# Performance work log

Hardware: AMD Instinct MI355X
Metric: run time of the kernel (lower is better)

The kernel has to match this reference:

```python
import jax, jax.numpy as jnp
from jax import lax
import numpy as np

B, S, D, H = 256, 2048, 16, 128
HH = H // 2  # head hidden = 64


def _p(key, shape, scale=0.05):
    return scale * jax.random.normal(key, shape, dtype=jnp.float32)


def setup_inputs() -> dict:
    key = jax.random.key(0)
    ks = jax.random.split(key, 12)
    return {
        "x": jax.random.normal(ks[0], (B, S, D), dtype=jnp.float32),
        # LSTM layer 0 (PyTorch gate order: i, f, g, o along the 4H axis)
        "W_ih0": _p(ks[1], (4 * H, D)),
        "W_hh0": _p(ks[2], (4 * H, H)),
        "b_ih0": jnp.zeros((4 * H,), jnp.float32),
        "b_hh0": jnp.zeros((4 * H,), jnp.float32),
        # LSTM layer 1
        "W_ih1": _p(ks[3], (4 * H, H)),
        "W_hh1": _p(ks[4], (4 * H, H)),
        "b_ih1": jnp.zeros((4 * H,), jnp.float32),
        "b_hh1": jnp.zeros((4 * H,), jnp.float32),
        # return head: Linear(H, H//2) -> LeakyReLU -> Linear(H//2, 1)
        "Wr1": _p(ks[5], (HH, H)), "br1": jnp.zeros((HH,), jnp.float32),
        "Wr2": _p(ks[6], (1, HH)), "br2": jnp.zeros((1,), jnp.float32),
        # vol head: Linear -> LeakyReLU -> Linear -> Softplus
        "Wv1": _p(ks[7], (HH, H)), "bv1": jnp.zeros((HH,), jnp.float32),
        "Wv2": _p(ks[8], (1, HH)), "bv2": jnp.zeros((1,), jnp.float32),
    }


def _lstm_layer(x, W_ih, W_hh, b_ih, b_hh):
    # x: (B, S, Din) -> hs: (B, S, H); PyTorch gate order i, f, g, o
    b, s, _ = x.shape
    h_dim = W_hh.shape[1]
    xg = jnp.einsum('bsd,gd->bsg', x, W_ih) + (b_ih + b_hh)  # (B, S, 4H)

    def step(carry, xg_t):
        h, c = carry
        g = xg_t + h @ W_hh.T
        i, f, gc, o = jnp.split(g, 4, axis=-1)
        i = jax.nn.sigmoid(i)
        f = jax.nn.sigmoid(f)
        gc = jnp.tanh(gc)
        o = jax.nn.sigmoid(o)
        c = f * c + i * gc
        h = o * jnp.tanh(c)
        return (h, c), h

    h0 = jnp.zeros((b, h_dim), x.dtype)
    (hN, cN), hs = lax.scan(step, (h0, jnp.zeros_like(h0)), jnp.swapaxes(xg, 0, 1))
    return jnp.swapaxes(hs, 0, 1), hN, cN


def reference(x, W_ih0, W_hh0, b_ih0, b_hh0, W_ih1, W_hh1, b_ih1, b_hh1,
              Wr1, br1, Wr2, br2, Wv1, bv1, Wv2, bv2):
    h1, hN0, cN0 = _lstm_layer(x, W_ih0, W_hh0, b_ih0, b_hh0)
    # inter-layer dropout is inactive at inference (eval mode)
    h2, hN1, cN1 = _lstm_layer(h1, W_ih1, W_hh1, b_ih1, b_hh1)
    # return head
    r = jax.nn.leaky_relu(jnp.einsum('bsh,kh->bsk', h2, Wr1) + br1)
    returns = jnp.einsum('bsk,ok->bso', r, Wr2) + br2
    # volatility head
    v = jax.nn.leaky_relu(jnp.einsum('bsh,kh->bsk', h2, Wv1) + bv1)
    volatility = jax.nn.softplus(jnp.einsum('bsk,ok->bso', v, Wv2) + bv2)
    hidden_h = jnp.stack([hN0, hN1], axis=0)  # (num_layers, B, H)
    hidden_c = jnp.stack([cN0, cN1], axis=0)
    return returns, volatility, hidden_h, hidden_c
```

## Files before the change

kernel.cpp:

```cpp
#include <hip/hip_runtime.h>
#include <hip/hip_bf16.h>

#define B_ 256
#define S_ 2048
#define D_ 16
#define H_ 128

typedef unsigned int u32;
typedef unsigned short u16;
typedef _Float16 h2t __attribute__((ext_vector_type(2)));

#define RET0 ((size_t)0)
#define VOL0 ((size_t)524288)
#define HH0  ((size_t)1048576)
#define HC0  ((size_t)1114112)

__device__ __forceinline__ float fdot2(u32 a, u32 b, float c) {
    return __builtin_amdgcn_fdot2(__builtin_bit_cast(h2t, a),
                                  __builtin_bit_cast(h2t, b), c, false);
}
__device__ __forceinline__ u32 packh2(float a, float b) {
    h2t h; h[0] = (_Float16)a; h[1] = (_Float16)b;
    return __builtin_bit_cast(u32, h);
}
__device__ __forceinline__ float sigm(float x) {
    return __builtin_amdgcn_rcpf(1.f + __builtin_amdgcn_exp2f(-1.44269504f * x));
}
__device__ __forceinline__ float tanh_(float x) {
    return 2.f * __builtin_amdgcn_rcpf(1.f + __builtin_amdgcn_exp2f(-2.88539008f * x)) - 1.f;
}
__device__ __forceinline__ float softplus_(float x) {
    if (x > 20.f) return x;
    const float e = __builtin_amdgcn_exp2f(1.44269504f * x);
    return 0.69314718f * __builtin_amdgcn_logf(1.f + e);
}

__global__ __launch_bounds__(512) void k_l0(
    const float* __restrict__ x, const float* __restrict__ Wih,
    const float* __restrict__ Whh, const float* __restrict__ bih,
    const float* __restrict__ bhh, u32* __restrict__ h1out,
    float* __restrict__ out)
{
    __shared__ float xs[512 * 16];
    __shared__ float gates[4][128];
    __shared__ float hf[128];
    __shared__ u32 och[64 * 64];

    const int tid = threadIdx.x, b = blockIdx.x;
    const int g = tid >> 7, m = tid & 127, row = g * 128 + m;

    float wx[16], wh[128];
#pragma unroll
    for (int j = 0; j < 16; ++j) wx[j] = Wih[row * 16 + j];
#pragma unroll
    for (int j = 0; j < 128; ++j) wh[j] = Whh[row * 128 + j];
    const float bs = bih[row] + bhh[row];

    float c = 0.f;
    if (tid < 128) hf[tid] = 0.f;
    __syncthreads();

    const float* xb = x + (size_t)b * S_ * D_;
    for (int t = 0; t < S_; ++t) {
        if ((t & 511) == 0) {
            for (int i = tid; i < 2048; i += 512) {
                const float4 v = *(const float4*)(xb + (size_t)t * 16 + i * 4);
                *(float4*)(&xs[i * 4]) = v;
            }
            __syncthreads();
        }
        float a = bs;
        const float* xt = &xs[(t & 511) * 16];
#pragma unroll
        for (int j = 0; j < 16; ++j) a += wx[j] * xt[j];
#pragma unroll
        for (int j = 0; j < 128; ++j) a += wh[j] * hf[j];
        gates[g][m] = a;
        __syncthreads();
        if (tid < 128) {
            const float ig = sigm(gates[0][tid]);
            const float fg = sigm(gates[1][tid]);
            const float gc = tanh_(gates[2][tid]);
            const float og = sigm(gates[3][tid]);
            c = fg * c + ig * gc;
            const float h = og * tanh_(c);
            hf[tid] = h;
            if (t == S_ - 1) {
                out[HH0 + (size_t)b * H_ + tid] = h;
                out[HC0 + (size_t)b * H_ + tid] = c;
            }
        }
        __syncthreads();
        if (tid < 64) och[(t & 63) * 64 + tid] = packh2(hf[2 * tid], hf[2 * tid + 1]);
        if ((t & 63) == 63) {
            __syncthreads();
            u32* dst = h1out + ((size_t)b * S_ + (t - 63)) * 64;
            *(uint4*)(dst + tid * 8)     = *(const uint4*)(&och[tid * 8]);
            *(uint4*)(dst + tid * 8 + 4) = *(const uint4*)(&och[tid * 8 + 4]);
        }
        __syncthreads();
    }
}

__global__ __launch_bounds__(512) void k_l1(
    u32* __restrict__ hws,
    const float* __restrict__ Wih, const float* __restrict__ Whh,
    const float* __restrict__ bih, const float* __restrict__ bhh,
    float* __restrict__ out)
{
    __shared__ u32 h1w[128 * 64];
    __shared__ float gates[4][128];
    __shared__ u32 hp[64];
    __shared__ u32 och[64 * 64];

    const int tid = threadIdx.x, b = blockIdx.x;
    const int g = tid >> 7, m = tid & 127, row = g * 128 + m;

    u32 wi[64], wh[64];
#pragma unroll
    for (int j = 0; j < 64; ++j) {
        const float2 a = *(const float2*)(Wih + row * 128 + 2 * j);
        const float2 cc = *(const float2*)(Whh + row * 128 + 2 * j);
        wi[j] = packh2(a.x, a.y);
        wh[j] = packh2(cc.x, cc.y);
    }
    const float bs = bih[row] + bhh[row];

    float c = 0.f;
    if (tid < 64) hp[tid] = 0u;
    __syncthreads();

    u32* hb = hws + (size_t)b * S_ * 64;
    for (int t = 0; t < S_; ++t) {
        if ((t & 127) == 0) {
            for (int i = tid; i < 2048; i += 512)
                *(uint4*)(&h1w[i * 4]) = *(const uint4*)(hb + (size_t)t * 64 + i * 4);
            __syncthreads();
        }
        float a = bs;
        const u32* h1t = &h1w[(t & 127) * 64];
#pragma unroll
        for (int j = 0; j < 64; ++j) a = fdot2(h1t[j], wi[j], a);
#pragma unroll
        for (int j = 0; j < 64; ++j) a = fdot2(hp[j], wh[j], a);
        gates[g][m] = a;
        __syncthreads();
        if (tid < 128) {
            const float ig = sigm(gates[0][tid]);
            const float fg = sigm(gates[1][tid]);
            const float gc = tanh_(gates[2][tid]);
            const float og = sigm(gates[3][tid]);
            c = fg * c + ig * gc;
            const float h = og * tanh_(c);
            ((u16*)hp)[tid] = __builtin_bit_cast(unsigned short, (_Float16)h);
            if (t == S_ - 1) {
                out[HH0 + 32768 + (size_t)b * H_ + tid] = h;
                out[HC0 + 32768 + (size_t)b * H_ + tid] = c;
            }
        }
        __syncthreads();
        if (tid < 64) och[(t & 63) * 64 + tid] = hp[tid];
        if ((t & 63) == 63) {
            __syncthreads();
            u32* dst = hb + (size_t)(t - 63) * 64;
            *(uint4*)(dst + tid * 8)     = *(const uint4*)(&och[tid * 8]);
            *(uint4*)(dst + tid * 8 + 4) = *(const uint4*)(&och[tid * 8 + 4]);
        }
        __syncthreads();
    }
}

__global__ __launch_bounds__(256) void k_heads(
    const u32* __restrict__ h2p,
    const float* __restrict__ Wr1, const float* __restrict__ br1,
    const float* __restrict__ Wr2, const float* __restrict__ br2,
    const float* __restrict__ Wv1, const float* __restrict__ bv1,
    const float* __restrict__ Wv2, const float* __restrict__ bv2,
    float* __restrict__ out)
{
    __shared__ u32 wr[64 * 64], wv[64 * 64];
    __shared__ float w2r[64], w2v[64], b1r[64], b1v[64];

    const int tid = threadIdx.x;
    for (int i = tid; i < 4096; i += 256) {
        wr[i] = packh2(Wr1[2 * i], Wr1[2 * i + 1]);
        wv[i] = packh2(Wv1[2 * i], Wv1[2 * i + 1]);
    }
    if (tid < 64) {
        w2r[tid] = Wr2[tid]; w2v[tid] = Wv2[tid];
        b1r[tid] = br1[tid]; b1v[tid] = bv1[tid];
    }
    __syncthreads();

    const size_t bs = (size_t)blockIdx.x * 256 + tid;
    u32 hq[64];
    const u32* src = h2p + bs * 64;
#pragma unroll
    for (int j4 = 0; j4 < 16; ++j4) {
        const uint4 v = *(const uint4*)(src + j4 * 4);
        hq[j4 * 4] = v.x; hq[j4 * 4 + 1] = v.y; hq[j4 * 4 + 2] = v.z; hq[j4 * 4 + 3] = v.w;
    }
    float ret = br2[0], vol = bv2[0];
    for (int k = 0; k < 64; ++k) {
        float r = b1r[k], v = b1v[k];
#pragma unroll
        for (int j = 0; j < 64; ++j) r = fdot2(hq[j], wr[k * 64 + j], r);
#pragma unroll
        for (int j = 0; j < 64; ++j) v = fdot2(hq[j], wv[k * 64 + j], v);
        r = r > 0.f ? r : 0.01f * r;
        v = v > 0.f ? v : 0.01f * v;
        ret += r * w2r[k];
        vol += v * w2v[k];
    }
    out[RET0 + bs] = ret;
    out[VOL0 + bs] = softplus_(vol);
}

extern "C" void kernel_launch(void* const* d_in, const int* in_sizes, int n_in,
                              void* d_out, int out_size, void* d_ws, size_t ws_size,
                              hipStream_t stream) {
    (void)in_sizes; (void)n_in; (void)out_size; (void)ws_size;
    const float* x    = (const float*)d_in[0];
    const float* Wih0 = (const float*)d_in[1];
    const float* Whh0 = (const float*)d_in[2];
    const float* bih0 = (const float*)d_in[3];
    const float* bhh0 = (const float*)d_in[4];
    const float* Wih1 = (const float*)d_in[5];
    const float* Whh1 = (const float*)d_in[6];
    const float* bih1 = (const float*)d_in[7];
    const float* bhh1 = (const float*)d_in[8];
    const float* Wr1  = (const float*)d_in[9];
    const float* br1  = (const float*)d_in[10];
    const float* Wr2  = (const float*)d_in[11];
    const float* br2  = (const float*)d_in[12];
    const float* Wv1  = (const float*)d_in[13];
    const float* bv1  = (const float*)d_in[14];
    const float* Wv2  = (const float*)d_in[15];
    const float* bv2  = (const float*)d_in[16];
    u32* hws = (u32*)d_ws;
    float* out = (float*)d_out;

    k_l0<<<B_, 512, 0, stream>>>(x, Wih0, Whh0, bih0, bhh0, hws, out);
    k_l1<<<B_, 512, 0, stream>>>(hws, Wih1, Whh1, bih1, bhh1, out);
    k_heads<<<2048, 256, 0, stream>>>(hws, Wr1, br1, Wr2, br2, Wv1, bv1, Wv2, bv2, out);
}
```

Measured before the change: 4.117 ms.

## Split gate rows across 8-lane groups, shuffle-reduce gates, cut barriers per step

```diff
diff --git a/kernel.cpp b/kernel.cpp
--- a/kernel.cpp
+++ b/kernel.cpp
@@ -35,138 +35,180 @@
     return 0.69314718f * __builtin_amdgcn_logf(1.f + e);
 }
 
-__global__ __launch_bounds__(512) void k_l0(
+__global__ __launch_bounds__(1024, 4) void k_l0(
     const float* __restrict__ x, const float* __restrict__ Wih,
     const float* __restrict__ Whh, const float* __restrict__ bih,
     const float* __restrict__ bhh, u32* __restrict__ h1out,
     float* __restrict__ out)
 {
-    __shared__ float xs[512 * 16];
-    __shared__ float gates[4][128];
-    __shared__ float hf[128];
-    __shared__ u32 och[64 * 64];
+    __shared__ u32 xp2[2][4096];
+    __shared__ u32 hb[2][64];
+    __shared__ u32 och[4096];
 
     const int tid = threadIdx.x, b = blockIdx.x;
-    const int g = tid >> 7, m = tid & 127, row = g * 128 + m;
-
-    float wx[16], wh[128];
-#pragma unroll
-    for (int j = 0; j < 16; ++j) wx[j] = Wih[row * 16 + j];
-#pragma unroll
-    for (int j = 0; j < 128; ++j) wh[j] = Whh[row * 128 + j];
-    const float bs = bih[row] + bhh[row];
-
+    const int m = tid >> 3, g = (tid >> 1) & 3, k0 = tid & 1;
+    const int row = g * H_ + m;
+
+    u32 w[36];
+    {
+        const float* p1 = k0 ? (Whh + row * H_ + 56) : (Wih + row * D_);
+        const float* p2 = k0 ? (Whh + row * H_ + 72) : (Whh + row * H_);
+#pragma unroll
+        for (int j = 0; j < 4; ++j) {
+            const float4 f = ((const float4*)p1)[j];
+            w[2 * j] = packh2(f.x, f.y); w[2 * j + 1] = packh2(f.z, f.w);
+        }
+#pragma unroll
+        for (int j = 0; j < 14; ++j) {
+            const float4 f = ((const float4*)p2)[j];
+            w[8 + 2 * j] = packh2(f.x, f.y); w[9 + 2 * j] = packh2(f.z, f.w);
+        }
+    }
+    const float bs = k0 ? 0.f : (bih[row] + bhh[row]);
+
+    const float* xb = x + (size_t)b * S_ * D_;
+    for (int i = tid; i < 2048; i += 1024) {
+        const float4 v = *(const float4*)(xb + i * 4);
+        xp2[0][2 * i] = packh2(v.x, v.y);
+        xp2[0][2 * i + 1] = packh2(v.z, v.w);
+    }
+    if (tid < 128) ((u32*)hb)[tid] = 0u;
     float c = 0.f;
-    if (tid < 128) hf[tid] = 0.f;
     __syncthreads();
 
-    const float* xb = x + (size_t)b * S_ * D_;
     for (int t = 0; t < S_; ++t) {
-        if ((t & 511) == 0) {
-            for (int i = tid; i < 2048; i += 512) {
-                const float4 v = *(const float4*)(xb + (size_t)t * 16 + i * 4);
-                *(float4*)(&xs[i * 4]) = v;
+        if ((t & 511) == 0 && t < S_ - 512) {
+            const int nw = (t >> 9) + 1;
+            u32* dst = xp2[nw & 1];
+            const float* src = xb + (size_t)nw * 8192;
+            for (int i = tid; i < 2048; i += 1024) {
+                const float4 v = *(const float4*)(src + i * 4);
+                dst[2 * i] = packh2(v.x, v.y);
+                dst[2 * i + 1] = packh2(v.z, v.w);
             }
+        }
+        const u32* hprev = hb[(t + 1) & 1];
+        const u32* xslot = &xp2[(t >> 9) & 1][(t & 511) * 8];
+        const uint4* pA = (const uint4*)(k0 ? hprev + 28 : xslot);
+        const uint4* pB = (const uint4*)(k0 ? hprev + 36 : hprev);
+
+        float a0 = bs, a1 = 0.f, a2 = 0.f, a3 = 0.f;
+        {
+            const uint4 v0 = pA[0], v1 = pA[1];
+            a0 = fdot2(v0.x, w[0], a0); a1 = fdot2(v0.y, w[1], a1);
+            a2 = fdot2(v0.z, w[2], a2); a3 = fdot2(v0.w, w[3], a3);
+            a0 = fdot2(v1.x, w[4], a0); a1 = fdot2(v1.y, w[5], a1);
+            a2 = fdot2(v1.z, w[6], a2); a3 = fdot2(v1.w, w[7], a3);
+        }
+#pragma unroll
+        for (int p = 0; p < 7; ++p) {
+            const uint4 v = pB[p];
+            a0 = fdot2(v.x, w[8 + 4 * p], a0); a1 = fdot2(v.y, w[9 + 4 * p], a1);
+            a2 = fdot2(v.z, w[10 + 4 * p], a2); a3 = fdot2(v.w, w[11 + 4 * p], a3);
+        }
+        float a = (a0 + a1) + (a2 + a3);
+        a += __shfl_xor(a, 1);
+        const float af = __shfl_down(a, 2);
+        const float ag = __shfl_down(a, 4);
+        const float ao = __shfl_down(a, 6);
+        float hv = 0.f;
+        if ((tid & 7) == 0) {
+            const float ig = sigm(a), fg = sigm(af);
+            const float gc = tanh_(ag), og = sigm(ao);
+            c = fg * c + ig * gc;
+            hv = og * tanh_(c);
+        }
+        const float hnb = __shfl_down(hv, 8);
+        if ((tid & 15) == 0) {
+            const u32 pp = packh2(hv, hnb);
+            hb[t & 1][m >> 1] = pp;
+            och[(t & 63) * 64 + (m >> 1)] = pp;
+        }
+        if (t == S_ - 1 && (tid & 7) == 0) {
+            out[HH0 + (size_t)b * H_ + m] = hv;
+            out[HC0 + (size_t)b * H_ + m] = c;
+        }
+        __syncthreads();
+        if ((t & 63) == 63) {
+            u32* dst = h1out + ((size_t)b * S_ + (t - 63)) * 64;
+            *(uint4*)(dst + tid * 4) = *(const uint4*)(&och[tid * 4]);
             __syncthreads();
         }
-        float a = bs;
-        const float* xt = &xs[(t & 511) * 16];
-#pragma unroll
-        for (int j = 0; j < 16; ++j) a += wx[j] * xt[j];
-#pragma unroll
-        for (int j = 0; j < 128; ++j) a += wh[j] * hf[j];
-        gates[g][m] = a;
-        __syncthreads();
-        if (tid < 128) {
-            const float ig = sigm(gates[0][tid]);
-            const float fg = sigm(gates[1][tid]);
-            const float gc = tanh_(gates[2][tid]);
-            const float og = sigm(gates[3][tid]);
-            c = fg * c + ig * gc;
-            const float h = og * tanh_(c);
-            hf[tid] = h;
-            if (t == S_ - 1) {
-                out[HH0 + (size_t)b * H_ + tid] = h;
-                out[HC0 + (size_t)b * H_ + tid] = c;
-            }
-        }
-        __syncthreads();
-        if (tid < 64) och[(t & 63) * 64 + tid] = packh2(hf[2 * tid], hf[2 * tid + 1]);
-        if ((t & 63) == 63) {
-            __syncthreads();
-            u32* dst = h1out + ((size_t)b * S_ + (t - 63)) * 64;
-            *(uint4*)(dst + tid * 8)     = *(const uint4*)(&och[tid * 8]);
-            *(uint4*)(dst + tid * 8 + 4) = *(const uint4*)(&och[tid * 8 + 4]);
-        }
-        __syncthreads();
-    }
-}
-
-__global__ __launch_bounds__(512) void k_l1(
+    }
+}
+
+__global__ __launch_bounds__(1024, 4) void k_l1(
     u32* __restrict__ hws,
     const float* __restrict__ Wih, const float* __restrict__ Whh,
     const float* __restrict__ bih, const float* __restrict__ bhh,
     float* __restrict__ out)
 {
-    __shared__ u32 h1w[128 * 64];
-    __shared__ float gates[4][128];
-    __shared__ u32 hp[64];
-    __shared__ u32 och[64 * 64];
+    __shared__ u32 h1w[8192];
+    __shared__ u32 hp[2][64];
+    __shared__ u32 och[4096];
 
     const int tid = threadIdx.x, b = blockIdx.x;
-    const int g = tid >> 7, m = tid & 127, row = g * 128 + m;
-
-    u32 wi[64], wh[64];
-#pragma unroll
-    for (int j = 0; j < 64; ++j) {
-        const float2 a = *(const float2*)(Wih + row * 128 + 2 * j);
-        const float2 cc = *(const float2*)(Whh + row * 128 + 2 * j);
-        wi[j] = packh2(a.x, a.y);
-        wh[j] = packh2(cc.x, cc.y);
-    }
-    const float bs = bih[row] + bhh[row];
-
+    const int m = tid >> 3, g = (tid >> 1) & 3, k0 = tid & 1;
+    const int row = g * H_ + m;
+
+    u32 w[64];
+    {
+        const float4* ws_ = (const float4*)((k0 ? Whh : Wih) + row * H_);
+#pragma unroll
+        for (int j = 0; j < 32; ++j) {
+            const float4 f = ws_[j];
+            w[2 * j] = packh2(f.x, f.y); w[2 * j + 1] = packh2(f.z, f.w);
+        }
+    }
+    const float bs = k0 ? 0.f : (bih[row] + bhh[row]);
+
+    if (tid < 128) ((u32*)hp)[tid] = 0u;
     float c = 0.f;
-    if (tid < 64) hp[tid] = 0u;
     __syncthreads();
 
-    u32* hb = hws + (size_t)b * S_ * 64;
-    for (int t = 0; t < S_; ++t) {
-        if ((t & 127) == 0) {
-            for (int i = tid; i < 2048; i += 512)
-                *(uint4*)(&h1w[i * 4]) = *(const uint4*)(hb + (size_t)t * 64 + i * 4);
+    u32* hbase = hws + (size_t)b * S_ * 64;
+    for (int u = 0; u < S_; ++u) {
+        if ((u & 127) == 0) {
+            for (int i = tid; i < 2048; i += 1024)
+                *(uint4*)(&h1w[i * 4]) = *(const uint4*)(hbase + (size_t)u * 64 + i * 4);
             __syncthreads();
         }
-        float a = bs;
-        const u32* h1t = &h1w[(t & 127) * 64];
-#pragma unroll
-        for (int j = 0; j < 64; ++j) a = fdot2(h1t[j], wi[j], a);
-#pragma unroll
-        for (int j = 0; j < 64; ++j) a = fdot2(hp[j], wh[j], a);
-        gates[g][m] = a;
+        const uint4* src = (const uint4*)(k0 ? hp[(u + 1) & 1] : &h1w[(u & 127) * 64]);
+        float a0 = bs, a1 = 0.f, a2 = 0.f, a3 = 0.f;
+#pragma unroll
+        for (int p = 0; p < 16; ++p) {
+            const uint4 v = src[p];
+            a0 = fdot2(v.x, w[4 * p], a0); a1 = fdot2(v.y, w[4 * p + 1], a1);
+            a2 = fdot2(v.z, w[4 * p + 2], a2); a3 = fdot2(v.w, w[4 * p + 3], a3);
+        }
+        float a = (a0 + a1) + (a2 + a3);
+        a += __shfl_xor(a, 1);
+        const float af = __shfl_down(a, 2);
+        const float ag = __shfl_down(a, 4);
+        const float ao = __shfl_down(a, 6);
+        float hv = 0.f;
+        if ((tid & 7) == 0) {
+            const float ig = sigm(a), fg = sigm(af);
+            const float gc = tanh_(ag), og = sigm(ao);
+            c = fg * c + ig * gc;
+            hv = og * tanh_(c);
+        }
+        const float hnb = __shfl_down(hv, 8);
+        if ((tid & 15) == 0) {
+            const u32 pp = packh2(hv, hnb);
+            hp[u & 1][m >> 1] = pp;
+            och[(u & 63) * 64 + (m >> 1)] = pp;
+        }
+        if (u == S_ - 1 && (tid & 7) == 0) {
+            out[HH0 + 32768 + (size_t)b * H_ + m] = hv;
+            out[HC0 + 32768 + (size_t)b * H_ + m] = c;
+        }
         __syncthreads();
-        if (tid < 128) {
-            const float ig = sigm(gates[0][tid]);
-            const float fg = sigm(gates[1][tid]);
-            const float gc = tanh_(gates[2][tid]);
-            const float og = sigm(gates[3][tid]);
-            c = fg * c + ig * gc;
-            const float h = og * tanh_(c);
-            ((u16*)hp)[tid] = __builtin_bit_cast(unsigned short, (_Float16)h);
-            if (t == S_ - 1) {
-                out[HH0 + 32768 + (size_t)b * H_ + tid] = h;
-                out[HC0 + 32768 + (size_t)b * H_ + tid] = c;
-            }
-        }
-        __syncthreads();
-        if (tid < 64) och[(t & 63) * 64 + tid] = hp[tid];
-        if ((t & 63) == 63) {
+        if ((u & 63) == 63) {
+            u32* dst = hbase + (size_t)(u - 63) * 64;
+            *(uint4*)(dst + tid * 4) = *(const uint4*)(&och[tid * 4]);
             __syncthreads();
-            u32* dst = hb + (size_t)(t - 63) * 64;
-            *(uint4*)(dst + tid * 8)     = *(const uint4*)(&och[tid * 8]);
-            *(uint4*)(dst + tid * 8 + 4) = *(const uint4*)(&och[tid * 8 + 4]);
-        }
-        __syncthreads();
+        }
     }
 }
 
@@ -240,7 +282,7 @@
     u32* hws = (u32*)d_ws;
     float* out = (float*)d_out;
 
-    k_l0<<<B_, 512, 0, stream>>>(x, Wih0, Whh0, bih0, bhh0, hws, out);
-    k_l1<<<B_, 512, 0, stream>>>(hws, Wih1, Whh1, bih1, bhh1, out);
+    k_l0<<<B_, 1024, 0, stream>>>(x, Wih0, Whh0, bih0, bhh0, hws, out);
+    k_l1<<<B_, 1024, 0, stream>>>(hws, Wih1, Whh1, bih1, bhh1, out);
     k_heads<<<2048, 256, 0, stream>>>(hws, Wr1, br1, Wr2, br2, Wv1, bv1, Wv2, bv2, out);
 }
```

Measured after the change: 5.058 ms. +22.8%, slower.

## Batch LSTM recurrences across 16 sequences per block using MFMA

Applied to the files above, without the earlier changes.

```diff
diff --git a/kernel.cpp b/kernel.cpp
--- a/kernel.cpp
+++ b/kernel.cpp
@@ -9,19 +9,25 @@
 typedef unsigned int u32;
 typedef unsigned short u16;
 typedef _Float16 h2t __attribute__((ext_vector_type(2)));
+typedef _Float16 f16x8 __attribute__((ext_vector_type(8)));
+typedef float f32x4 __attribute__((ext_vector_type(4)));
 
 #define RET0 ((size_t)0)
 #define VOL0 ((size_t)524288)
 #define HH0  ((size_t)1048576)
 #define HC0  ((size_t)1114112)
 
-__device__ __forceinline__ float fdot2(u32 a, u32 b, float c) {
-    return __builtin_amdgcn_fdot2(__builtin_bit_cast(h2t, a),
-                                  __builtin_bit_cast(h2t, b), c, false);
-}
+#define MFMA16(a, b, c) __builtin_amdgcn_mfma_f32_16x16x32_f16(a, b, c, 0, 0, 0)
+
 __device__ __forceinline__ u32 packh2(float a, float b) {
     h2t h; h[0] = (_Float16)a; h[1] = (_Float16)b;
     return __builtin_bit_cast(u32, h);
+}
+__device__ __forceinline__ f16x8 pk8(float4 a, float4 b) {
+    f16x8 r;
+    r[0] = (_Float16)a.x; r[1] = (_Float16)a.y; r[2] = (_Float16)a.z; r[3] = (_Float16)a.w;
+    r[4] = (_Float16)b.x; r[5] = (_Float16)b.y; r[6] = (_Float16)b.z; r[7] = (_Float16)b.w;
+    return r;
 }
 __device__ __forceinline__ float sigm(float x) {
     return __builtin_amdgcn_rcpf(1.f + __builtin_amdgcn_exp2f(-1.44269504f * x));
@@ -34,139 +40,185 @@
     const float e = __builtin_amdgcn_exp2f(1.44269504f * x);
     return 0.69314718f * __builtin_amdgcn_logf(1.f + e);
 }
-
-__global__ __launch_bounds__(512) void k_l0(
+__device__ __forceinline__ float4 ld4(const float* p) { return *(const float4*)p; }
+
+
+__global__ __launch_bounds__(512, 2) void k_l0m(
     const float* __restrict__ x, const float* __restrict__ Wih,
     const float* __restrict__ Whh, const float* __restrict__ bih,
-    const float* __restrict__ bhh, u32* __restrict__ h1out,
+    const float* __restrict__ bhh, u32* __restrict__ hws,
     float* __restrict__ out)
 {
-    __shared__ float xs[512 * 16];
-    __shared__ float gates[4][128];
-    __shared__ float hf[128];
-    __shared__ u32 och[64 * 64];
-
-    const int tid = threadIdx.x, b = blockIdx.x;
-    const int g = tid >> 7, m = tid & 127, row = g * 128 + m;
-
-    float wx[16], wh[128];
-#pragma unroll
-    for (int j = 0; j < 16; ++j) wx[j] = Wih[row * 16 + j];
-#pragma unroll
-    for (int j = 0; j < 128; ++j) wh[j] = Whh[row * 128 + j];
-    const float bs = bih[row] + bhh[row];
-
-    float c = 0.f;
-    if (tid < 128) hf[tid] = 0.f;
+    __shared__ u32 ring[8192];
+
+    const int tid = threadIdx.x, g = blockIdx.x;
+    const int l = tid & 63, w = tid >> 6;
+    const int ub = w * 16;
+    const int col = l & 15, kg = l >> 4;
+
+    f16x8 wB[4][5];
+    float bias[4];
+#pragma unroll
+    for (int gt = 0; gt < 4; ++gt) {
+        const int n = gt * 128 + ub + col;
+        if (kg < 2) {
+            const float* p = Wih + n * 16 + kg * 8;
+            wB[gt][0] = pk8(ld4(p), ld4(p + 4));
+        } else {
+            f16x8 z = {0, 0, 0, 0, 0, 0, 0, 0};
+            wB[gt][0] = z;
+        }
+#pragma unroll
+        for (int kt = 1; kt < 5; ++kt) {
+            const float* p = Whh + n * 128 + (kt - 1) * 32 + kg * 8;
+            wB[gt][kt] = pk8(ld4(p), ld4(p + 4));
+        }
+        bias[gt] = bih[n] + bhh[n];
+    }
+
+    for (int i = tid; i < 8192; i += 512) ring[i] = 0;
+    float c1[4] = {0.f, 0.f, 0.f, 0.f};
     __syncthreads();
 
-    const float* xb = x + (size_t)b * S_ * D_;
+    const float* xrow = x + ((size_t)(g * 16 + col) * S_) * D_;
     for (int t = 0; t < S_; ++t) {
-        if ((t & 511) == 0) {
-            for (int i = tid; i < 2048; i += 512) {
-                const float4 v = *(const float4*)(xb + (size_t)t * 16 + i * 4);
-                *(float4*)(&xs[i * 4]) = v;
+        f16x8 ax = {0, 0, 0, 0, 0, 0, 0, 0};
+        if (kg < 2) {
+            const float* xp = xrow + t * 16 + kg * 8;
+            ax = pk8(ld4(xp), ld4(xp + 4));
+        }
+        f16x8 ah[4];
+        {
+            const int sl = ((t - 1) & 7) << 10;
+#pragma unroll
+            for (int kt = 0; kt < 4; ++kt)
+                ah[kt] = __builtin_bit_cast(f16x8,
+                    *(const uint4*)&ring[sl + col * 64 + (((kt * 4 + kg) ^ (col & 7)) << 2)]);
+        }
+        f32x4 acc[4];
+#pragma unroll
+        for (int gt = 0; gt < 4; ++gt) {
+            f32x4 a = {bias[gt], bias[gt], bias[gt], bias[gt]};
+            a = MFMA16(ax, wB[gt][0], a);
+#pragma unroll
+            for (int kt = 1; kt < 5; ++kt) a = MFMA16(ah[kt - 1], wB[gt][kt], a);
+            acc[gt] = a;
+        }
+#pragma unroll
+        for (int j = 0; j < 4; ++j) {
+            const float ai = acc[0][j], af = acc[1][j], ag = acc[2][j], ao = acc[3][j];
+            c1[j] = sigm(af) * c1[j] + sigm(ai) * tanh_(ag);
+            const float h = sigm(ao) * tanh_(c1[j]);
+            const u32 hp = packh2(h, __shfl_down(h, 1));
+            const int r = kg * 4 + j;
+            if (!(l & 1)) {
+                const int p = (ub + col) >> 1;
+                ring[((t & 7) << 10) + r * 64 + ((((p >> 2)) ^ (r & 7)) << 2) + (p & 3)] = hp;
+            }
+            if (t == S_ - 1) {
+                const size_t b = g * 16 + r;
+                out[HH0 + b * H_ + ub + col] = h;
+                out[HC0 + b * H_ + ub + col] = c1[j];
+            }
+        }
+        __syncthreads();
+        if ((t & 7) == 7) {
+#pragma unroll
+            for (int q = 0; q < 4; ++q) {
+                const int ch = tid * 4 + q;
+                const int s = ch >> 8, rr = (ch >> 4) & 15, cc = ch & 15;
+                const uint4 v = *(const uint4*)&ring[(s << 10) + rr * 64 + ((cc ^ (rr & 7)) << 2)];
+                *(uint4*)(hws + (((size_t)g * S_ + (t - 7 + s)) * 16 + rr) * 64 + cc * 4) = v;
             }
             __syncthreads();
         }
-        float a = bs;
-        const float* xt = &xs[(t & 511) * 16];
-#pragma unroll
-        for (int j = 0; j < 16; ++j) a += wx[j] * xt[j];
-#pragma unroll
-        for (int j = 0; j < 128; ++j) a += wh[j] * hf[j];
-        gates[g][m] = a;
-        __syncthreads();
-        if (tid < 128) {
-            const float ig = sigm(gates[0][tid]);
-            const float fg = sigm(gates[1][tid]);
-            const float gc = tanh_(gates[2][tid]);
-            const float og = sigm(gates[3][tid]);
-            c = fg * c + ig * gc;
-            const float h = og * tanh_(c);
-            hf[tid] = h;
-            if (t == S_ - 1) {
-                out[HH0 + (size_t)b * H_ + tid] = h;
-                out[HC0 + (size_t)b * H_ + tid] = c;
-            }
-        }
-        __syncthreads();
-        if (tid < 64) och[(t & 63) * 64 + tid] = packh2(hf[2 * tid], hf[2 * tid + 1]);
-        if ((t & 63) == 63) {
-            __syncthreads();
-            u32* dst = h1out + ((size_t)b * S_ + (t - 63)) * 64;
-            *(uint4*)(dst + tid * 8)     = *(const uint4*)(&och[tid * 8]);
-            *(uint4*)(dst + tid * 8 + 4) = *(const uint4*)(&och[tid * 8 + 4]);
-        }
-        __syncthreads();
-    }
-}
-
-__global__ __launch_bounds__(512) void k_l1(
+    }
+}
+
+__global__ __launch_bounds__(512, 2) void k_l1m(
     u32* __restrict__ hws,
     const float* __restrict__ Wih, const float* __restrict__ Whh,
     const float* __restrict__ bih, const float* __restrict__ bhh,
     float* __restrict__ out)
 {
-    __shared__ u32 h1w[128 * 64];
-    __shared__ float gates[4][128];
-    __shared__ u32 hp[64];
-    __shared__ u32 och[64 * 64];
-
-    const int tid = threadIdx.x, b = blockIdx.x;
-    const int g = tid >> 7, m = tid & 127, row = g * 128 + m;
-
-    u32 wi[64], wh[64];
-#pragma unroll
-    for (int j = 0; j < 64; ++j) {
-        const float2 a = *(const float2*)(Wih + row * 128 + 2 * j);
-        const float2 cc = *(const float2*)(Whh + row * 128 + 2 * j);
-        wi[j] = packh2(a.x, a.y);
-        wh[j] = packh2(cc.x, cc.y);
-    }
-    const float bs = bih[row] + bhh[row];
-
-    float c = 0.f;
-    if (tid < 64) hp[tid] = 0u;
+    __shared__ u32 ring[8192];
+
+    const int tid = threadIdx.x, g = blockIdx.x;
+    const int l = tid & 63, w = tid >> 6;
+    const int ub = w * 16;
+    const int col = l & 15, kg = l >> 4;
+
+    f16x8 wB[4][8];
+    float bias[4];
+#pragma unroll
+    for (int gt = 0; gt < 4; ++gt) {
+        const int n = gt * 128 + ub + col;
+#pragma unroll
+        for (int kt = 0; kt < 8; ++kt) {
+            const float* p = ((kt < 4) ? Wih : Whh) + n * 128 + (kt & 3) * 32 + kg * 8;
+            wB[gt][kt] = pk8(ld4(p), ld4(p + 4));
+        }
+        bias[gt] = bih[n] + bhh[n];
+    }
+
+    for (int i = tid; i < 8192; i += 512) ring[i] = 0;
+    float c2[4] = {0.f, 0.f, 0.f, 0.f};
     __syncthreads();
 
-    u32* hb = hws + (size_t)b * S_ * 64;
-    for (int t = 0; t < S_; ++t) {
-        if ((t & 127) == 0) {
-            for (int i = tid; i < 2048; i += 512)
-                *(uint4*)(&h1w[i * 4]) = *(const uint4*)(hb + (size_t)t * 64 + i * 4);
+    for (int u = 0; u < S_; ++u) {
+        f16x8 a1[4];
+        {
+            const u32* hrow = hws + (((size_t)g * S_ + u) * 16 + col) * 64;
+#pragma unroll
+            for (int kt = 0; kt < 4; ++kt)
+                a1[kt] = __builtin_bit_cast(f16x8, *(const uint4*)(hrow + kt * 16 + kg * 4));
+        }
+        f16x8 a2[4];
+        {
+            const int sl = ((u - 1) & 7) << 10;
+#pragma unroll
+            for (int kt = 0; kt < 4; ++kt)
+                a2[kt] = __builtin_bit_cast(f16x8,
+                    *(const uint4*)&ring[sl + col * 64 + (((kt * 4 + kg) ^ (col & 7)) << 2)]);
+        }
+        f32x4 acc[4];
+#pragma unroll
+        for (int gt = 0; gt < 4; ++gt) {
+            f32x4 a = {bias[gt], bias[gt], bias[gt], bias[gt]};
+#pragma unroll
+            for (int kt = 0; kt < 4; ++kt) a = MFMA16(a1[kt], wB[gt][kt], a);
+#pragma unroll
+            for (int kt = 4; kt < 8; ++kt) a = MFMA16(a2[kt - 4], wB[gt][kt], a);
+            acc[gt] = a;
+        }
+#pragma unroll
+        for (int j = 0; j < 4; ++j) {
+            const float ai = acc[0][j], af = acc[1][j], ag = acc[2][j], ao = acc[3][j];
+            c2[j] = sigm(af) * c2[j] + sigm(ai) * tanh_(ag);
+            const float h = sigm(ao) * tanh_(c2[j]);
+            const u32 hp = packh2(h, __shfl_down(h, 1));
+            const int r = kg * 4 + j;
+            if (!(l & 1)) {
+                const int p = (ub + col) >> 1;
+                ring[((u & 7) << 10) + r * 64 + ((((p >> 2)) ^ (r & 7)) << 2) + (p & 3)] = hp;
+            }
+            if (u == S_ - 1) {
+                const size_t b = g * 16 + r;
+                out[HH0 + 32768 + b * H_ + ub + col] = h;
+                out[HC0 + 32768 + b * H_ + ub + col] = c2[j];
+            }
+        }
+        __syncthreads();
+        if ((u & 7) == 7) {
+#pragma unroll
+            for (int q = 0; q < 4; ++q) {
+                const int ch = tid * 4 + q;
+                const int s = ch >> 8, rr = (ch >> 4) & 15, cc = ch & 15;
+                const uint4 v = *(const uint4*)&ring[(s << 10) + rr * 64 + ((cc ^ (rr & 7)) << 2)];
+                *(uint4*)(hws + (((size_t)g * S_ + (u - 7 + s)) * 16 + rr) * 64 + cc * 4) = v;
+            }
             __syncthreads();
         }
-        float a = bs;
-        const u32* h1t = &h1w[(t & 127) * 64];
-#pragma unroll
-        for (int j = 0; j < 64; ++j) a = fdot2(h1t[j], wi[j], a);
-#pragma unroll
-        for (int j = 0; j < 64; ++j) a = fdot2(hp[j], wh[j], a);
-        gates[g][m] = a;
-        __syncthreads();
-        if (tid < 128) {
-            const float ig = sigm(gates[0][tid]);
-            const float fg = sigm(gates[1][tid]);
-            const float gc = tanh_(gates[2][tid]);
-            const float og = sigm(gates[3][tid]);
-            c = fg * c + ig * gc;
-            const float h = og * tanh_(c);
-            ((u16*)hp)[tid] = __builtin_bit_cast(unsigned short, (_Float16)h);
-            if (t == S_ - 1) {
-                out[HH0 + 32768 + (size_t)b * H_ + tid] = h;
-                out[HC0 + 32768 + (size_t)b * H_ + tid] = c;
-            }
-        }
-        __syncthreads();
-        if (tid < 64) och[(t & 63) * 64 + tid] = hp[tid];
-        if ((t & 63) == 63) {
-            __syncthreads();
-            u32* dst = hb + (size_t)(t - 63) * 64;
-            *(uint4*)(dst + tid * 8)     = *(const uint4*)(&och[tid * 8]);
-            *(uint4*)(dst + tid * 8 + 4) = *(const uint4*)(&och[tid * 8 + 4]);
-        }
-        __syncthreads();
     }
 }
 
@@ -192,9 +244,13 @@
     }
     __syncthreads();
 
-    const size_t bs = (size_t)blockIdx.x * 256 + tid;
+    const int g = blockIdx.x >> 7;
+    const int s = (blockIdx.x & 127) * 16 + (tid >> 4);
+    const int r = tid & 15;
+    const int b = g * 16 + r;
+
     u32 hq[64];
-    const u32* src = h2p + bs * 64;
+    const u32* src = h2p + (((size_t)g * S_ + s) * 16 + r) * 64;
 #pragma unroll
     for (int j4 = 0; j4 < 16; ++j4) {
         const uint4 v = *(const uint4*)(src + j4 * 4);
@@ -202,18 +258,21 @@
     }
     float ret = br2[0], vol = bv2[0];
     for (int k = 0; k < 64; ++k) {
-        float r = b1r[k], v = b1v[k];
-#pragma unroll
-        for (int j = 0; j < 64; ++j) r = fdot2(hq[j], wr[k * 64 + j], r);
-#pragma unroll
-        for (int j = 0; j < 64; ++j) v = fdot2(hq[j], wv[k * 64 + j], v);
-        r = r > 0.f ? r : 0.01f * r;
-        v = v > 0.f ? v : 0.01f * v;
-        ret += r * w2r[k];
-        vol += v * w2v[k];
-    }
-    out[RET0 + bs] = ret;
-    out[VOL0 + bs] = softplus_(vol);
+        float rr = b1r[k], vv = b1v[k];
+#pragma unroll
+        for (int j = 0; j < 64; ++j) {
+            rr = __builtin_amdgcn_fdot2(__builtin_bit_cast(h2t, hq[j]),
+                                        __builtin_bit_cast(h2t, wr[k * 64 + j]), rr, false);
+            vv = __builtin_amdgcn_fdot2(__builtin_bit_cast(h2t, hq[j]),
+                                        __builtin_bit_cast(h2t, wv[k * 64 + j]), vv, false);
+        }
+        rr = rr > 0.f ? rr : 0.01f * rr;
+        vv = vv > 0.f ? vv : 0.01f * vv;
+        ret += rr * w2r[k];
+        vol += vv * w2v[k];
+    }
+    out[RET0 + (size_t)b * S_ + s] = ret;
+    out[VOL0 + (size_t)b * S_ + s] = softplus_(vol);
 }
 
 extern "C" void kernel_launch(void* const* d_in, const int* in_sizes, int n_in,
@@ -237,10 +296,11 @@
     const float* bv1  = (const float*)d_in[14];
     const float* Wv2  = (const float*)d_in[15];
     const float* bv2  = (const float*)d_in[16];
-    u32* hws = (u32*)d_ws;
+    u32* hws  = (u32*)d_ws;
     float* out = (float*)d_out;
 
-    k_l0<<<B_, 512, 0, stream>>>(x, Wih0, Whh0, bih0, bhh0, hws, out);
-    k_l1<<<B_, 512, 0, stream>>>(hws, Wih1, Whh1, bih1, bhh1, out);
-    k_heads<<<2048, 256, 0, stream>>>(hws, Wr1, br1, Wr2, br2, Wv1, bv1, Wv2, bv2, out);
-}
+    k_l0m<<<16, 512, 0, stream>>>(x, Wih0, Whh0, bih0, bhh0, hws, out);
+    k_l1m<<<16, 512, 0, stream>>>(hws, Wih1, Whh1, bih1, bhh1, out);
+    k_heads<<<2048, 256, 0, stream>>>(hws, Wr1, br1, Wr2, br2,
+                                      Wv1, bv1, Wv2, bv2, out);
+}
```

Result: slower. 7.340 ms (+78.3%).

## Split LSTM gate matvec across K-slices with one barrier per step

Applied to the files above, without the earlier changes.

```diff
diff --git a/kernel.cpp b/kernel.cpp
--- a/kernel.cpp
+++ b/kernel.cpp
@@ -7,7 +7,6 @@
 #define H_ 128
 
 typedef unsigned int u32;
-typedef unsigned short u16;
 typedef _Float16 h2t __attribute__((ext_vector_type(2)));
 
 #define RET0 ((size_t)0)
@@ -34,139 +33,243 @@
     const float e = __builtin_amdgcn_exp2f(1.44269504f * x);
     return 0.69314718f * __builtin_amdgcn_logf(1.f + e);
 }
-
-__global__ __launch_bounds__(512) void k_l0(
+__device__ __forceinline__ float dnb1(float a) {
+    return __builtin_bit_cast(float, __builtin_amdgcn_update_dpp(
+        0, __builtin_bit_cast(int, a), 0xB1, 0xF, 0xF, true));
+}
+
+__global__ __launch_bounds__(512, 2) void k_l0(
     const float* __restrict__ x, const float* __restrict__ Wih,
     const float* __restrict__ Whh, const float* __restrict__ bih,
     const float* __restrict__ bhh, u32* __restrict__ h1out,
     float* __restrict__ out)
 {
-    __shared__ float xs[512 * 16];
-    __shared__ float gates[4][128];
-    __shared__ float hf[128];
-    __shared__ u32 och[64 * 64];
+    __shared__ u32 xp2[2][2048];
+    __shared__ float gates[2][4][128][4];
+    __shared__ u32 hb[8][16];
+    __shared__ u32 och[2][2048];
 
     const int tid = threadIdx.x, b = blockIdx.x;
-    const int g = tid >> 7, m = tid & 127, row = g * 128 + m;
-
-    float wx[16], wh[128];
-#pragma unroll
-    for (int j = 0; j < 16; ++j) wx[j] = Wih[row * 16 + j];
-#pragma unroll
-    for (int j = 0; j < 128; ++j) wh[j] = Whh[row * 128 + j];
-    const float bs = bih[row] + bhh[row];
-
+    const int ksl = tid >> 7, m = tid & 127;
+    const int wv = tid >> 6, j = tid & 63;
+    const int unit = (ksl << 5) + (j & 31);
+
+    u32 wx[8], wh[64];
+#pragma unroll
+    for (int g = 0; g < 4; ++g) {
+        const int row = g * H_ + m;
+        const float4 fx = *(const float4*)(Wih + row * D_ + ksl * 4);
+        wx[g * 2]     = packh2(fx.x, fx.y);
+        wx[g * 2 + 1] = packh2(fx.z, fx.w);
+        const float4* whr = (const float4*)(Whh + row * H_ + ksl * 32);
+#pragma unroll
+        for (int q = 0; q < 8; ++q) {
+            const float4 f = whr[q];
+            wh[g * 16 + 2 * q]     = packh2(f.x, f.y);
+            wh[g * 16 + 2 * q + 1] = packh2(f.z, f.w);
+        }
+    }
+    const float bias0 = bih[unit] + bhh[unit];
+    const float bias1 = bih[128 + unit] + bhh[128 + unit];
+    const float bias2 = bih[256 + unit] + bhh[256 + unit];
+    const float bias3 = bih[384 + unit] + bhh[384 + unit];
+
+    const float* xb = x + (size_t)b * S_ * D_;
+#pragma unroll
+    for (int k = 0; k < 2; ++k) {
+        const int i = tid + k * 512;
+        const float4 v = *(const float4*)(xb + i * 4);
+        xp2[0][2 * i]     = packh2(v.x, v.y);
+        xp2[0][2 * i + 1] = packh2(v.z, v.w);
+    }
+    if (tid < 128) ((u32*)hb)[tid] = 0u;
     float c = 0.f;
-    if (tid < 128) hf[tid] = 0.f;
-    __syncthreads();
-
-    const float* xb = x + (size_t)b * S_ * D_;
+    __syncthreads();
+
     for (int t = 0; t < S_; ++t) {
-        if ((t & 511) == 0) {
-            for (int i = tid; i < 2048; i += 512) {
-                const float4 v = *(const float4*)(xb + (size_t)t * 16 + i * 4);
-                *(float4*)(&xs[i * 4]) = v;
+        if ((t & 255) == 0 && t < S_ - 256) {
+            const int nw = (t >> 8) + 1;
+#pragma unroll
+            for (int k = 0; k < 2; ++k) {
+                const int i = tid + k * 512;
+                const float4 v = *(const float4*)(xb + (size_t)nw * 4096 + i * 4);
+                xp2[nw & 1][2 * i]     = packh2(v.x, v.y);
+                xp2[nw & 1][2 * i + 1] = packh2(v.z, v.w);
             }
-            __syncthreads();
-        }
-        float a = bs;
-        const float* xt = &xs[(t & 511) * 16];
-#pragma unroll
-        for (int j = 0; j < 16; ++j) a += wx[j] * xt[j];
-#pragma unroll
-        for (int j = 0; j < 128; ++j) a += wh[j] * hf[j];
-        gates[g][m] = a;
+        }
+        const uint2 xv = *(const uint2*)&xp2[(t >> 8) & 1][(t & 255) * 8 + ksl * 2];
+        const uint4* hq = (const uint4*)hb[wv];
+        const uint4 h0 = hq[0], h1 = hq[1], h2 = hq[2], h3 = hq[3];
+        float a0 = fdot2(xv.x, wx[0], 0.f); a0 = fdot2(xv.y, wx[1], a0);
+        float a1 = fdot2(xv.x, wx[2], 0.f); a1 = fdot2(xv.y, wx[3], a1);
+        float a2 = fdot2(xv.x, wx[4], 0.f); a2 = fdot2(xv.y, wx[5], a2);
+        float a3 = fdot2(xv.x, wx[6], 0.f); a3 = fdot2(xv.y, wx[7], a3);
+#define DG(vv, p)                                                              \
+        a0 = fdot2(vv, wh[p], a0);        a1 = fdot2(vv, wh[16 + (p)], a1);    \
+        a2 = fdot2(vv, wh[32 + (p)], a2); a3 = fdot2(vv, wh[48 + (p)], a3);
+        DG(h0.x, 0) DG(h0.y, 1) DG(h0.z, 2) DG(h0.w, 3)
+        DG(h1.x, 4) DG(h1.y, 5) DG(h1.z, 6) DG(h1.w, 7)
+        DG(h2.x, 8) DG(h2.y, 9) DG(h2.z, 10) DG(h2.w, 11)
+        DG(h3.x, 12) DG(h3.y, 13) DG(h3.z, 14) DG(h3.w, 15)
+#undef DG
+        float4 part; part.x = a0; part.y = a1; part.z = a2; part.w = a3;
+        *(float4*)&gates[t & 1][ksl][m][0] = part;
         __syncthreads();
-        if (tid < 128) {
-            const float ig = sigm(gates[0][tid]);
-            const float fg = sigm(gates[1][tid]);
-            const float gc = tanh_(gates[2][tid]);
-            const float og = sigm(gates[3][tid]);
-            c = fg * c + ig * gc;
-            const float h = og * tanh_(c);
-            hf[tid] = h;
-            if (t == S_ - 1) {
-                out[HH0 + (size_t)b * H_ + tid] = h;
-                out[HC0 + (size_t)b * H_ + tid] = c;
-            }
-        }
-        __syncthreads();
-        if (tid < 64) och[(t & 63) * 64 + tid] = packh2(hf[2 * tid], hf[2 * tid + 1]);
-        if ((t & 63) == 63) {
-            __syncthreads();
-            u32* dst = h1out + ((size_t)b * S_ + (t - 63)) * 64;
-            *(uint4*)(dst + tid * 8)     = *(const uint4*)(&och[tid * 8]);
-            *(uint4*)(dst + tid * 8 + 4) = *(const uint4*)(&och[tid * 8 + 4]);
-        }
-        __syncthreads();
-    }
-}
-
-__global__ __launch_bounds__(512) void k_l1(
+        if ((t & 31) == 0 && t) {
+            u32* dst = h1out + ((size_t)b * S_ + (t - 32)) * 64;
+            *(uint4*)(dst + tid * 4) = *(const uint4*)&och[((t >> 5) & 1) ^ 1][tid * 4];
+        }
+        const float4 s0 = *(const float4*)&gates[t & 1][0][unit][0];
+        const float4 s1 = *(const float4*)&gates[t & 1][1][unit][0];
+        const float4 s2 = *(const float4*)&gates[t & 1][2][unit][0];
+        const float4 s3 = *(const float4*)&gates[t & 1][3][unit][0];
+        const float ig = sigm((s0.x + s1.x) + (s2.x + s3.x) + bias0);
+        const float fg = sigm((s0.y + s1.y) + (s2.y + s3.y) + bias1);
+        const float gc = tanh_((s0.z + s1.z) + (s2.z + s3.z) + bias2);
+        const float og = sigm((s0.w + s1.w) + (s2.w + s3.w) + bias3);
+        c = fg * c + ig * gc;
+        const float h = og * tanh_(c);
+        const u32 pp = packh2(h, dnb1(h));
+        if ((j & 33) == 0) {
+            hb[wv][j >> 1] = pp;
+            if (!(wv & 1)) och[(t >> 5) & 1][(t & 31) * 64 + (unit >> 1)] = pp;
+        }
+        if (t == S_ - 1 && !(wv & 1) && j < 32) {
+            out[HH0 + (size_t)b * H_ + unit] = h;
+            out[HC0 + (size_t)b * H_ + unit] = c;
+        }
+    }
+    __syncthreads();
+    {
+        u32* dst = h1out + ((size_t)b * S_ + (S_ - 32)) * 64;
+        *(uint4*)(dst + tid * 4) = *(const uint4*)&och[1][tid * 4];
+    }
+}
+
+__global__ __launch_bounds__(512, 2) void k_l1(
     u32* __restrict__ hws,
     const float* __restrict__ Wih, const float* __restrict__ Whh,
     const float* __restrict__ bih, const float* __restrict__ bhh,
     float* __restrict__ out)
 {
-    __shared__ u32 h1w[128 * 64];
-    __shared__ float gates[4][128];
-    __shared__ u32 hp[64];
-    __shared__ u32 och[64 * 64];
+    __shared__ u32 h1w[2][5120];
+    __shared__ float gates[2][4][128][4];
+    __shared__ u32 hb[8][32];
+    __shared__ u32 och[2][2048];
 
     const int tid = threadIdx.x, b = blockIdx.x;
-    const int g = tid >> 7, m = tid & 127, row = g * 128 + m;
-
-    u32 wi[64], wh[64];
-#pragma unroll
-    for (int j = 0; j < 64; ++j) {
-        const float2 a = *(const float2*)(Wih + row * 128 + 2 * j);
-        const float2 cc = *(const float2*)(Whh + row * 128 + 2 * j);
-        wi[j] = packh2(a.x, a.y);
-        wh[j] = packh2(cc.x, cc.y);
-    }
-    const float bs = bih[row] + bhh[row];
-
+    const int ksl = tid >> 7, m = tid & 127;
+    const int wv = tid >> 6, j = tid & 63;
+    const int unit = ((ksl & 1) << 6) + j;
+
+    u32 w[128];
+    const float* Wsel = (ksl < 2) ? Wih : Whh;
+    const int eb = (ksl & 1) * 64;
+#pragma unroll
+    for (int g = 0; g < 4; ++g) {
+        const int row = g * H_ + m;
+        const float4* wr_ = (const float4*)(Wsel + row * H_ + eb);
+#pragma unroll
+        for (int q = 0; q < 16; ++q) {
+            const float4 f = wr_[q];
+            w[g * 32 + 2 * q]     = packh2(f.x, f.y);
+            w[g * 32 + 2 * q + 1] = packh2(f.z, f.w);
+        }
+    }
+    const float bias0 = bih[unit] + bhh[unit];
+    const float bias1 = bih[128 + unit] + bhh[128 + unit];
+    const float bias2 = bih[256 + unit] + bhh[256 + unit];
+    const float bias3 = bih[384 + unit] + bhh[384 + unit];
+
+    u32* hbase = hws + (size_t)b * S_ * 64;
+#pragma unroll
+    for (int k = 0; k < 2; ++k) {
+        const int i = tid + k * 512;
+        const uint4 v = *(const uint4*)(hbase + i * 4);
+        *(uint4*)&h1w[0][(i >> 4) * 80 + ((i & 15) >> 2) * 20 + (i & 3) * 4] = v;
+    }
+    if (tid < 256) ((u32*)hb)[tid] = 0u;
     float c = 0.f;
-    if (tid < 64) hp[tid] = 0u;
-    __syncthreads();
-
-    u32* hb = hws + (size_t)b * S_ * 64;
-    for (int t = 0; t < S_; ++t) {
-        if ((t & 127) == 0) {
-            for (int i = tid; i < 2048; i += 512)
-                *(uint4*)(&h1w[i * 4]) = *(const uint4*)(hb + (size_t)t * 64 + i * 4);
-            __syncthreads();
-        }
-        float a = bs;
-        const u32* h1t = &h1w[(t & 127) * 64];
-#pragma unroll
-        for (int j = 0; j < 64; ++j) a = fdot2(h1t[j], wi[j], a);
-#pragma unroll
-        for (int j = 0; j < 64; ++j) a = fdot2(hp[j], wh[j], a);
-        gates[g][m] = a;
+    __syncthreads();
+
+    for (int u = 0; u < S_; ++u) {
+        uint4 v0, v1, v2, v3, v4, v5, v6, v7;
+        if (ksl < 2) {
+            const u32* src = &h1w[(u >> 6) & 1][(u & 63) * 80 + ksl * 40];
+            v0 = *(const uint4*)(src);      v1 = *(const uint4*)(src + 4);
+            v2 = *(const uint4*)(src + 8);  v3 = *(const uint4*)(src + 12);
+            v4 = *(const uint4*)(src + 20); v5 = *(const uint4*)(src + 24);
+            v6 = *(const uint4*)(src + 28); v7 = *(const uint4*)(src + 32);
+        } else {
+            const u32* src = hb[wv];
+            v0 = *(const uint4*)(src);      v1 = *(const uint4*)(src + 4);
+            v2 = *(const uint4*)(src + 8);  v3 = *(const uint4*)(src + 12);
+            v4 = *(const uint4*)(src + 16); v5 = *(const uint4*)(src + 20);
+            v6 = *(const uint4*)(src + 24); v7 = *(const uint4*)(src + 28);
+        }
+        float a0 = 0.f, a1 = 0.f, a2 = 0.f, a3 = 0.f;
+#define DQ(vv, q4)                                                             \
+        a0 = fdot2(vv.x, w[q4], a0);          a0 = fdot2(vv.y, w[(q4)+1], a0); \
+        a0 = fdot2(vv.z, w[(q4)+2], a0);      a0 = fdot2(vv.w, w[(q4)+3], a0); \
+        a1 = fdot2(vv.x, w[32+(q4)], a1);     a1 = fdot2(vv.y, w[33+(q4)], a1);\
+        a1 = fdot2(vv.z, w[34+(q4)], a1);     a1 = fdot2(vv.w, w[35+(q4)], a1);\
+        a2 = fdot2(vv.x, w[64+(q4)], a2);     a2 = fdot2(vv.y, w[65+(q4)], a2);\
+        a2 = fdot2(vv.z, w[66+(q4)], a2);     a2 = fdot2(vv.w, w[67+(q4)], a2);\
+        a3 = fdot2(vv.x, w[96+(q4)], a3);     a3 = fdot2(vv.y, w[97+(q4)], a3);\
+        a3 = fdot2(vv.z, w[98+(q4)], a3);     a3 = fdot2(vv.w, w[99+(q4)], a3);
+        DQ(v0, 0) DQ(v1, 4) DQ(v2, 8) DQ(v3, 12)
+        DQ(v4, 16) DQ(v5, 20) DQ(v6, 24) DQ(v7, 28)
+#undef DQ
+        float4 part; part.x = a0; part.y = a1; part.z = a2; part.w = a3;
+        *(float4*)&gates[u & 1][ksl][m][0] = part;
         __syncthreads();
-        if (tid < 128) {
-            const float ig = sigm(gates[0][tid]);
-            const float fg = sigm(gates[1][tid]);
-            const float gc = tanh_(gates[2][tid]);
-            const float og = sigm(gates[3][tid]);
+        if ((u & 31) == 0 && u && wv < 2) {
+            u32* dst = hbase + (size_t)(u - 32) * 64;
+            const u32* sb = och[((u >> 5) & 1) ^ 1];
+            const int t0 = tid & 127;
+#pragma unroll
+            for (int k = 0; k < 4; ++k)
+                *(uint4*)(dst + (t0 + k * 128) * 4) =
+                    *(const uint4*)(sb + (t0 + k * 128) * 4);
+        }
+        if ((u & 63) == 32 && u + 32 < S_ && wv < 2) {
+            const int nw = (u >> 6) + 1;
+            const u32* sw = hbase + (size_t)nw * 4096;
+            u32* dw = h1w[nw & 1];
+            const int t0 = tid & 127;
+#pragma unroll
+            for (int k = 0; k < 8; ++k) {
+                const int i = t0 + k * 128;
+                *(uint4*)&dw[(i >> 4) * 80 + ((i & 15) >> 2) * 20 + (i & 3) * 4] =
+                    *(const uint4*)(sw + i * 4);
+            }
+        }
+        if (ksl >= 2) {
+            const float4 s0 = *(const float4*)&gates[u & 1][0][unit][0];
+            const float4 s1 = *(const float4*)&gates[u & 1][1][unit][0];
+            const float4 s2 = *(const float4*)&gates[u & 1][2][unit][0];
+            const float4 s3 = *(const float4*)&gates[u & 1][3][unit][0];
+            const float ig = sigm((s0.x + s1.x) + (s2.x + s3.x) + bias0);
+            const float fg = sigm((s0.y + s1.y) + (s2.y + s3.y) + bias1);
+            const float gc = tanh_((s0.z + s1.z) + (s2.z + s3.z) + bias2);
+            const float og = sigm((s0.w + s1.w) + (s2.w + s3.w) + bias3);
             c = fg * c + ig * gc;
             const float h = og * tanh_(c);
-            ((u16*)hp)[tid] = __builtin_bit_cast(unsigned short, (_Float16)h);
-            if (t == S_ - 1) {
-                out[HH0 + 32768 + (size_t)b * H_ + tid] = h;
-                out[HC0 + 32768 + (size_t)b * H_ + tid] = c;
+            const u32 pp = packh2(h, dnb1(h));
+            if (!(j & 1)) {
+                hb[wv][j >> 1] = pp;
+                if (!(wv & 1)) och[(u >> 5) & 1][(u & 31) * 64 + (unit >> 1)] = pp;
             }
-        }
-        __syncthreads();
-        if (tid < 64) och[(t & 63) * 64 + tid] = hp[tid];
-        if ((t & 63) == 63) {
-            __syncthreads();
-            u32* dst = hb + (size_t)(t - 63) * 64;
-            *(uint4*)(dst + tid * 8)     = *(const uint4*)(&och[tid * 8]);
-            *(uint4*)(dst + tid * 8 + 4) = *(const uint4*)(&och[tid * 8 + 4]);
-        }
-        __syncthreads();
+            if (u == S_ - 1 && !(wv & 1)) {
+                out[HH0 + 32768 + (size_t)b * H_ + unit] = h;
+                out[HC0 + 32768 + (size_t)b * H_ + unit] = c;
+            }
+        }
+    }
+    __syncthreads();
+    {
+        u32* dst = hbase + (size_t)(S_ - 32) * 64;
+        *(uint4*)(dst + tid * 4) = *(const uint4*)&och[1][tid * 4];
     }
 }
 
@@ -198,7 +301,8 @@
 #pragma unroll
     for (int j4 = 0; j4 < 16; ++j4) {
         const uint4 v = *(const uint4*)(src + j4 * 4);
-        hq[j4 * 4] = v.x; hq[j4 * 4 + 1] = v.y; hq[j4 * 4 + 2] = v.z; hq[j4 * 4 + 3] = v.w;
+        hq[j4 * 4] = v.x; hq[j4 * 4 + 1] = v.y;
+        hq[j4 * 4 + 2] = v.z; hq[j4 * 4 + 3] = v.w;
     }
     float ret = br2[0], vol = bv2[0];
     for (int k = 0; k < 64; ++k) {
@@ -237,10 +341,11 @@
     const float* bv1  = (const float*)d_in[14];
     const float* Wv2  = (const float*)d_in[15];
     const float* bv2  = (const float*)d_in[16];
-    u32* hws = (u32*)d_ws;
+    u32* hws  = (u32*)d_ws;
     float* out = (float*)d_out;
 
     k_l0<<<B_, 512, 0, stream>>>(x, Wih0, Whh0, bih0, bhh0, hws, out);
     k_l1<<<B_, 512, 0, stream>>>(hws, Wih1, Whh1, bih1, bhh1, out);
-    k_heads<<<2048, 256, 0, stream>>>(hws, Wr1, br1, Wr2, br2, Wv1, bv1, Wv2, bv2, out);
-}
+    k_heads<<<2048, 256, 0, stream>>>(hws, Wr1, br1, Wr2, br2,
+                                      Wv1, bv1, Wv2, bv2, out);
+}
```

Measured after the change: 3.438 ms. 1.2x faster.
